# Performance work log

Hardware: AMD Instinct MI355X
Metric: run time of the kernel (lower is better)

The kernel has to match this reference:

```python
import jax, jax.numpy as jnp
import numpy as np

N_NODES = 50000
N_EDGES = 800000
F_IN = 32
H = 128
N_REL = 4
MAX_DEG = 10
N_GRAPHS = 64
N_BLOCKS = 2


def setup_inputs() -> dict:
    key = jax.random.key(0)
    ks = jax.random.split(key, 20)
    s = 0.05
    return {
        "x": jax.random.normal(ks[0], (N_NODES, F_IN), jnp.float32),
        "edge_index": jax.random.randint(ks[1], (2, N_EDGES), 0, N_NODES, dtype=jnp.int32),
        "edge_attr": jax.random.randint(ks[2], (N_EDGES,), 0, N_REL, dtype=jnp.int32),
        "batch_idx": jnp.sort(jax.random.randint(ks[3], (N_NODES,), 0, N_GRAPHS, dtype=jnp.int32)),
        "embed_W": jax.random.normal(ks[4], (F_IN, H), jnp.float32) * s,
        "embed_b": jax.random.normal(ks[5], (H,), jnp.float32) * s,
        "rgcn_Wrel": jax.random.normal(ks[6], (N_BLOCKS, N_REL, H, H), jnp.float32) * s,
        "rgcn_Wroot": jax.random.normal(ks[7], (N_BLOCKS, H, H), jnp.float32) * s,
        "rgcn_b": jax.random.normal(ks[8], (N_BLOCKS, H), jnp.float32) * s,
        "mf_Wl": jax.random.normal(ks[9], (N_BLOCKS, MAX_DEG + 1, H, H), jnp.float32) * s,
        "mf_bl": jax.random.normal(ks[10], (N_BLOCKS, MAX_DEG + 1, H), jnp.float32) * s,
        "mf_Wr": jax.random.normal(ks[11], (N_BLOCKS, MAX_DEG + 1, H, H), jnp.float32) * s,
        "lin1_W": jax.random.normal(ks[12], (H, H), jnp.float32) * s,
        "lin1_b": jax.random.normal(ks[13], (H,), jnp.float32) * s,
        "lin2_W": jax.random.normal(ks[14], (H, 1), jnp.float32) * s,
        "lin2_b": jax.random.normal(ks[15], (1,), jnp.float32) * s,
    }


def _rgcn(x, src, dst, rel, Wrel, Wroot, b):
    # PyG RGCNConv with default aggr='mean': per-relation mean over incoming
    # edges, then per-relation weight, plus root transform and bias.
    seg = dst * N_REL + rel  # composite segment id: (node, relation)
    agg = jax.ops.segment_sum(x[src], seg, num_segments=N_NODES * N_REL)
    cnt = jax.ops.segment_sum(jnp.ones((seg.shape[0],), x.dtype), seg,
                              num_segments=N_NODES * N_REL)
    agg = (agg / jnp.maximum(cnt, 1.0)[:, None]).reshape(N_NODES, N_REL, H)
    return jnp.einsum('nrh,rho->no', agg, Wrel) + x @ Wroot + b


def _mfconv(x, src, dst, Wl, bl, Wr):
    # PyG MFConv: sum-aggregate neighbors, then per-degree-bucket linear heads
    # (degree = in-degree clamped to MAX_DEG); lin_r applied to root x (no bias).
    h = jax.ops.segment_sum(x[src], dst, num_segments=N_NODES)  # [N,H]
    deg = jax.ops.segment_sum(jnp.ones((src.shape[0],), jnp.int32), dst,
                              num_segments=N_NODES)
    deg = jnp.minimum(deg, MAX_DEG)  # [N]
    # out_all: [D+1, N, H] candidate outputs, one per degree bucket
    out_all = (jnp.einsum('nh,dho->dno', h, Wl)
               + jnp.einsum('nh,dho->dno', x, Wr)
               + bl[:, None, :])
    return jnp.take_along_axis(out_all, deg[None, :, None], axis=0)[0]


def reference(x, edge_index, edge_attr, batch_idx, embed_W, embed_b,
              rgcn_Wrel, rgcn_Wroot, rgcn_b, mf_Wl, mf_bl, mf_Wr,
              lin1_W, lin1_b, lin2_W, lin2_b):
    src, dst = edge_index[0], edge_index[1]
    h = x @ embed_W + embed_b
    for blk in range(N_BLOCKS):
        if blk > 0:  # first block uses Identity instead of ReLU
            h = jax.nn.relu(h)
        h = _rgcn(h, src, dst, edge_attr, rgcn_Wrel[blk], rgcn_Wroot[blk], rgcn_b[blk])
        h = jax.nn.relu(h)
        h = _mfconv(h, src, dst, mf_Wl[blk], mf_bl[blk], mf_Wr[blk])
    g = jax.ops.segment_sum(h, batch_idx, num_segments=N_GRAPHS)  # global_add_pool
    g = jax.nn.relu(g @ lin1_W + lin1_b)
    return g @ lin2_W + lin2_b
```

## Files before the change

### kernel.cpp

```cpp
#include <hip/hip_runtime.h>
#include <hip/hip_bf16.h>

#define NRELS 4
#define MAXDEG 10
#define NBUCK 11
#define POOL_CHUNKS 8

typedef __attribute__((ext_vector_type(8))) short s16x8;
typedef __attribute__((ext_vector_type(4))) float f32x4;
typedef __attribute__((ext_vector_type(8))) unsigned short u16x8;

__device__ inline unsigned short f2b(float f) {
  __hip_bfloat16 h = __float2bfloat16(f);
  return *reinterpret_cast<unsigned short*>(&h);
}
__device__ inline float b2f(unsigned short u) {
  union { unsigned int i; float f; } v;
  v.i = ((unsigned int)u) << 16;
  return v.f;
}
__device__ inline float blo(unsigned int v) {
  union { unsigned int i; float f; } x;
  x.i = v << 16;
  return x.f;
}
__device__ inline float bhi(unsigned int v) {
  union { unsigned int i; float f; } x;
  x.i = v & 0xffff0000u;
  return x.f;
}

typedef __attribute__((address_space(3))) unsigned int lds_uint;
typedef __attribute__((address_space(1))) const unsigned int glob_uint;
__device__ __forceinline__ void gld_lds16(const void* g, void* l) {
  __builtin_amdgcn_global_load_lds((glob_uint*)g, (lds_uint*)l, 16, 0, 0);
}

__global__ __launch_bounds__(512) void coarse_count_scan(
    const int* __restrict__ dst, int* __restrict__ bhist, int* __restrict__ boff,
    int* __restrict__ bcur, int* __restrict__ done, int* __restrict__ perm, int permCap,
    int NB, int E, int nblocks) {
  __shared__ int lh[512];
  __shared__ int lastf;
  int t = threadIdx.x;
  lh[t] = 0;
  __syncthreads();
  for (int i = blockIdx.x * 512 + t; i < permCap; i += nblocks * 512) perm[i] = -1;
  int base = blockIdx.x * 4096;
  int lim = E - base;
  if (lim > 4096) lim = 4096;
  for (int i = t; i < lim; i += 512) atomicAdd(&lh[dst[base + i] >> 7], 1);
  __syncthreads();
  if (lh[t]) atomicAdd(&bhist[t], lh[t]);
  __threadfence();
  __syncthreads();
  if (t == 0) lastf = (atomicAdd(done, 1) == nblocks - 1) ? 1 : 0;
  __syncthreads();
  if (!lastf) return;
  int v = (t < NB) ? atomicAdd(&bhist[t], 0) : 0;
  lh[t] = v;
  __syncthreads();
  for (int o = 1; o < 512; o <<= 1) {
    int x = (t >= o) ? lh[t - o] : 0;
    __syncthreads();
    lh[t] += x;
    __syncthreads();
  }
  if (t < NB) {
    int st = lh[t] - v;
    boff[t] = st;
    bcur[t] = st;
  }
  if (t == 0) boff[NB] = E;
}

__global__ __launch_bounds__(512) void coarse_scatter(
    const int* __restrict__ src, const int* __restrict__ dst, const int* __restrict__ rel,
    int* __restrict__ bcur, uint2* __restrict__ ebuf, int E) {
  __shared__ int lhist[512];
  __shared__ int lstart[512];
  __shared__ int lcur[512];
  __shared__ int gbase[512];
  __shared__ uint2 stage[4096];
  int t = threadIdx.x;
  lhist[t] = 0;
  __syncthreads();
  int base = blockIdx.x * 4096;
  int lim = E - base;
  if (lim > 4096) lim = 4096;
  for (int i = t; i < lim; i += 512) atomicAdd(&lhist[dst[base + i] >> 7], 1);
  __syncthreads();
  int myc = lhist[t];
  lstart[t] = myc;
  __syncthreads();
  for (int o = 1; o < 512; o <<= 1) {
    int x = (t >= o) ? lstart[t - o] : 0;
    __syncthreads();
    lstart[t] += x;
    __syncthreads();
  }
  int incl = lstart[t];
  __syncthreads();
  lstart[t] = incl - myc;
  lcur[t] = 0;
  if (myc > 0) gbase[t] = atomicAdd(&bcur[t], myc);
  __syncthreads();
  for (int i = t; i < lim; i += 512) {
    int e = base + i;
    int d = dst[e];
    int b = d >> 7;
    int slot = lstart[b] + atomicAdd(&lcur[b], 1);
    stage[slot] = make_uint2((unsigned)(d * 4 + rel[e]), (unsigned)src[e]);
  }
  __syncthreads();
  for (int i = t; i < lim; i += 512) {
    uint2 val = stage[i];
    int b = (int)(val.x >> 9);
    ebuf[gbase[b] + (i - lstart[b])] = val;
  }
}

__global__ __launch_bounds__(512) void fine_place(
    const uint2* __restrict__ ebuf, const int* __restrict__ boff, int* __restrict__ cnt,
    int* __restrict__ seg_start, float* __restrict__ inv, int* __restrict__ deg,
    int* __restrict__ bucket, int* __restrict__ hist, int* __restrict__ csr, int NSEG) {
  __shared__ int lh[512];
  __shared__ int sc[512];
  __shared__ int lcur[512];
  __shared__ int lbh[16];
  int t = threadIdx.x;
  int b = blockIdx.x;
  lh[t] = 0;
  if (t < 16) lbh[t] = 0;
  __syncthreads();
  int s = boff[b], e = boff[b + 1];
  for (int i = s + t; i < e; i += 512) atomicAdd(&lh[ebuf[i].x & 511], 1);
  __syncthreads();
  int v = lh[t];
  sc[t] = v;
  __syncthreads();
  for (int o = 1; o < 512; o <<= 1) {
    int x = (t >= o) ? sc[t - o] : 0;
    __syncthreads();
    sc[t] += x;
    __syncthreads();
  }
  int gseg = b * 512 + t;
  int mystart = s + sc[t] - v;
  lcur[t] = mystart;
  if (gseg < NSEG) {
    cnt[gseg] = v;
    seg_start[gseg] = mystart;
    inv[gseg] = 1.0f / (float)(v > 1 ? v : 1);
    if ((t & 3) == 0) {
      int d = sc[t + 3] - sc[t] + v;
      int n = gseg >> 2;
      deg[n] = d;
      int bk = d < MAXDEG ? d : MAXDEG;
      bucket[n] = bk;
      atomicAdd(&lbh[bk], 1);
    }
  }
  __syncthreads();
  if (t < NBUCK && lbh[t]) atomicAdd(&hist[t], lbh[t]);
  for (int i = s + t; i < e; i += 512) {
    uint2 vv = ebuf[i];
    int pos = atomicAdd(&lcur[vv.x & 511], 1);
    csr[pos] = (int)vv.y;
  }
}

__global__ void build_perm(const int* __restrict__ bucket, const int* __restrict__ hist,
                           int* __restrict__ fill, int* __restrict__ perm, int N) {
  __shared__ int soff[NBUCK];
  if (threadIdx.x == 0) {
    int acc = 0;
    for (int b = 0; b < NBUCK; b++) {
      soff[b] = acc;
      acc += ((hist[b] + 63) >> 6) << 6;
    }
  }
  __syncthreads();
  int n = blockIdx.x * 256 + threadIdx.x;
  int b = (n < N) ? bucket[n] : -1;
  int lane = threadIdx.x & 63;
  for (int bb = 0; bb < NBUCK; bb++) {
    unsigned long long m = __ballot(b == bb);
    if (m == 0ULL) continue;
    int leader = __ffsll(m) - 1;
    int base = 0;
    if (lane == leader) base = atomicAdd(&fill[bb], __popcll(m));
    base = __shfl(base, leader);
    if (b == bb) {
      int idx = __popcll(m & ((1ULL << lane) - 1ULL));
      perm[soff[bb] + base + idx] = n;
    }
  }
}

__global__ __launch_bounds__(256) void embed_conv(
    const float* __restrict__ x, const float* __restrict__ embW,
    const float* __restrict__ bias, const float* __restrict__ Wrel,
    const float* __restrict__ Wroot, const float* __restrict__ Wl,
    const float* __restrict__ Wr, unsigned short* __restrict__ Bt,
    unsigned short* __restrict__ Btm, unsigned short* __restrict__ out, int N, int nbE) {
  if ((int)blockIdx.x >= nbE) {
    const int R1 = 2 * 128 * 640;
    const int R2 = R1 + 2 * 11 * 128 * 256;
    int t = (blockIdx.x - nbE) * 256 + threadIdx.x;
    if (t < R1) {
      int blk = t / 81920;
      int rem = t % 81920;
      int n = rem / 640;
      int k = rem % 640;
      float v;
      if (k < 512)
        v = Wrel[(size_t)blk * 65536 + (size_t)k * 128 + n];
      else
        v = Wroot[(size_t)blk * 16384 + (size_t)(k - 512) * 128 + n];
      Bt[t] = f2b(v);
    } else if (t < R2) {
      int t2 = t - R1;
      int k = t2 & 255;
      int n = (t2 >> 8) & 127;
      int bb = (t2 >> 15) % 11;
      int blk = t2 / (11 * 128 * 256);
      float v;
      if (k < 128)
        v = Wl[(((size_t)blk * 11 + bb) * 128 + k) * 128 + n];
      else
        v = Wr[(((size_t)blk * 11 + bb) * 128 + (k - 128)) * 128 + n];
      Btm[t2] = f2b(v);
    }
    return;
  }
  __shared__ unsigned char As[64 * 80];
  __shared__ unsigned char Bs[128 * 80];
  int t = threadIdx.x;
  int m0 = blockIdx.x * 64;
  {
    int r = t >> 2, s = t & 3;
    int gr = m0 + r;
    if (gr >= N) gr = N - 1;
    const float* xp = x + (size_t)gr * 32 + s * 8;
    float4 f0 = *(const float4*)xp;
    float4 f1 = *(const float4*)(xp + 4);
    u16x8 o;
    o[0] = f2b(f0.x); o[1] = f2b(f0.y); o[2] = f2b(f0.z); o[3] = f2b(f0.w);
    o[4] = f2b(f1.x); o[5] = f2b(f1.y); o[6] = f2b(f1.z); o[7] = f2b(f1.w);
    *(u16x8*)(As + r * 80 + s * 16) = o;
  }
  {
    int n = t >> 1, hf = t & 1;
    unsigned short tmp[16];
#pragma unroll
    for (int j = 0; j < 16; j++) tmp[j] = f2b(embW[(size_t)(hf * 16 + j) * 128 + n]);
    *(u16x8*)(Bs + n * 80 + hf * 32) = *(u16x8*)tmp;
    *(u16x8*)(Bs + n * 80 + hf * 32 + 16) = *(u16x8*)(tmp + 8);
  }
  __syncthreads();
  int lane = t & 63, wave = t >> 6;
  int row = lane & 15, quad = lane >> 4;
  int nh = wave * 32;
  f32x4 acc[2][4];
#pragma unroll
  for (int i = 0; i < 2; i++)
#pragma unroll
    for (int j = 0; j < 4; j++) acc[i][j] = (f32x4){0.f, 0.f, 0.f, 0.f};
  s16x8 af[4], bf[2];
#pragma unroll
  for (int mt = 0; mt < 4; mt++) {
    int R = mt * 16 + row;
    af[mt] = *(const s16x8*)(As + R * 80 + quad * 16);
  }
#pragma unroll
  for (int nt = 0; nt < 2; nt++) {
    int R = nh + nt * 16 + row;
    bf[nt] = *(const s16x8*)(Bs + R * 80 + quad * 16);
  }
#pragma unroll
  for (int nt = 0; nt < 2; nt++)
#pragma unroll
    for (int mt = 0; mt < 4; mt++)
      acc[nt][mt] = __builtin_amdgcn_mfma_f32_16x16x32_bf16(af[mt], bf[nt], acc[nt][mt], 0, 0, 0);
#pragma unroll
  for (int nt = 0; nt < 2; nt++) {
    int n = nh + nt * 16 + row;
    float bv = bias[n];
#pragma unroll
    for (int mt = 0; mt < 4; mt++) {
#pragma unroll
      for (int r4 = 0; r4 < 4; r4++) {
        int m = m0 + mt * 16 + quad * 4 + r4;
        if (m < N) out[(size_t)m * 128 + n] = f2b(acc[nt][mt][r4] + bv);
      }
    }
  }
}

__device__ __forceinline__ void acc8v(float* a, uint4 v) {
  a[0] += blo(v.x); a[1] += bhi(v.x);
  a[2] += blo(v.y); a[3] += bhi(v.y);
  a[4] += blo(v.z); a[5] += bhi(v.z);
  a[6] += blo(v.w); a[7] += bhi(v.w);
}

__device__ __forceinline__ void gather_seg(const unsigned short* __restrict__ hb,
                                           const int* __restrict__ csr, int st, int cn,
                                           int chunk, float* a) {
  const unsigned short* hq = hb + chunk * 16;
  int i = 0;
  for (; i + 2 <= cn; i += 2) {
    int p0 = csr[st + i], p1 = csr[st + i + 1];
    const uint4* r0 = (const uint4*)(hq + (size_t)p0 * 128);
    const uint4* r1 = (const uint4*)(hq + (size_t)p1 * 128);
    uint4 v00 = r0[0], v01 = r0[1];
    uint4 v10 = r1[0], v11 = r1[1];
    acc8v(a + 0, v00); acc8v(a + 8, v01);
    acc8v(a + 0, v10); acc8v(a + 8, v11);
  }
  if (i < cn) {
    const uint4* r0 = (const uint4*)(hq + (size_t)csr[st + i] * 128);
    acc8v(a + 0, r0[0]); acc8v(a + 8, r0[1]);
  }
}

__device__ __forceinline__ void write_frag(unsigned char* Ag, int ln, int chunk,
                                           const float* a, float w) {
  int s = chunk >> 2;
#pragma unroll
  for (int h = 0; h < 2; h++) {
    int c = (((chunk & 3) * 2 + h)) ^ (ln & 7);
    const float* p = a + h * 8;
    uint4 o;
    o.x = (unsigned int)f2b(p[0] * w) | ((unsigned int)f2b(p[1] * w) << 16);
    o.y = (unsigned int)f2b(p[2] * w) | ((unsigned int)f2b(p[3] * w) << 16);
    o.z = (unsigned int)f2b(p[4] * w) | ((unsigned int)f2b(p[5] * w) << 16);
    o.w = (unsigned int)f2b(p[6] * w) | ((unsigned int)f2b(p[7] * w) << 16);
    *(uint4*)(Ag + s * 8192 + ln * 128 + (c << 4)) = o;
  }
}

__device__ __forceinline__ void gemm_tile_gB(const unsigned char* Areg, const char* Bp,
                                             int strideB, int row, int quad, int nh,
                                             f32x4 acc[2][4]) {
#pragma unroll
  for (int s = 0; s < 2; s++) {
#pragma unroll
    for (int ks = 0; ks < 2; ks++) {
      int cch = ks * 4 + quad;
      s16x8 af[4], bf[2];
#pragma unroll
      for (int mt = 0; mt < 4; mt++) {
        int R = mt * 16 + row;
        af[mt] = *(const s16x8*)(Areg + s * 8192 + R * 128 + ((cch ^ (R & 7)) << 4));
      }
#pragma unroll
      for (int nt = 0; nt < 2; nt++) {
        int R = nh + nt * 16 + row;
        bf[nt] = *(const s16x8*)(Bp + (size_t)R * strideB + s * 128 + cch * 16);
      }
#pragma unroll
      for (int nt = 0; nt < 2; nt++)
#pragma unroll
        for (int mt = 0; mt < 4; mt++)
          acc[nt][mt] = __builtin_amdgcn_mfma_f32_16x16x32_bf16(af[mt], bf[nt], acc[nt][mt], 0, 0, 0);
    }
  }
}

__global__ __launch_bounds__(256) void rgcn_fused(
    const unsigned short* __restrict__ hb, const int* __restrict__ csr,
    const int* __restrict__ seg_start, const int* __restrict__ cnt,
    const float* __restrict__ inv, const int* __restrict__ perm,
    const unsigned short* __restrict__ Bt, const float* __restrict__ bias,
    unsigned short* __restrict__ out) {
  __shared__ unsigned char Ag0[16384];
  __shared__ unsigned char Ag1[16384];
  __shared__ int nodes[64];
  int t = threadIdx.x;
  int m0 = blockIdx.x * 64;
  if (t < 64) nodes[t] = perm[m0 + t];
  __syncthreads();
  int lane = t & 63, wave = t >> 6;
  int row = lane & 15, quad = lane >> 4;
  int nh = wave * 32;
  int chunk = t & 7, lnb = t >> 3;
  f32x4 acc[2][4];
#pragma unroll
  for (int i = 0; i < 2; i++)
#pragma unroll
    for (int j = 0; j < 4; j++) acc[i][j] = (f32x4){0.f, 0.f, 0.f, 0.f};

#pragma unroll
  for (int rp = 0; rp < 4; rp += 2) {
#pragma unroll
    for (int pp = 0; pp < 2; pp++) {
      int ln = pp * 32 + lnb;
      int nd = nodes[ln];
      float a0[16], a1[16];
#pragma unroll
      for (int j = 0; j < 16; j++) { a0[j] = 0.f; a1[j] = 0.f; }
      float w0 = 1.f, w1 = 1.f;
      if (nd >= 0) {
        int sb = nd * 4 + rp;
        int2 st2 = *(const int2*)(seg_start + sb);
        int2 cn2 = *(const int2*)(cnt + sb);
        float2 w2 = *(const float2*)(inv + sb);
        w0 = w2.x; w1 = w2.y;
        gather_seg(hb, csr, st2.x, cn2.x, chunk, a0);
        gather_seg(hb, csr, st2.y, cn2.y, chunk, a1);
      }
      write_frag(Ag0, ln, chunk, a0, w0);
      write_frag(Ag1, ln, chunk, a1, w1);
    }
    __syncthreads();
    gemm_tile_gB(Ag0, (const char*)Bt + rp * 256, 1280, row, quad, nh, acc);
    gemm_tile_gB(Ag1, (const char*)Bt + (rp + 1) * 256, 1280, row, quad, nh, acc);
    __syncthreads();
  }
#pragma unroll
  for (int s = 0; s < 2; s++)
#pragma unroll
    for (int p = 0; p < 2; p++) {
      int o = s * 8192 + p * 4096 + t * 16;
      int r = (o >> 7) & 63, c = ((o >> 4) & 7) ^ (r & 7);
      int nd = nodes[r];
      if (nd < 0) nd = 0;
      gld_lds16((const char*)hb + (size_t)nd * 256 + s * 128 + c * 16, Ag0 + o);
    }
  __syncthreads();
  gemm_tile_gB(Ag0, (const char*)Bt + 1024, 1280, row, quad, nh, acc);
#pragma unroll
  for (int nt = 0; nt < 2; nt++) {
    int n = nh + nt * 16 + row;
    float bv = bias[n];
#pragma unroll
    for (int mt = 0; mt < 4; mt++) {
#pragma unroll
      for (int r4 = 0; r4 < 4; r4++) {
        int nd = nodes[mt * 16 + quad * 4 + r4];
        if (nd >= 0) out[(size_t)nd * 128 + n] = f2b(fmaxf(acc[nt][mt][r4] + bv, 0.f));
      }
    }
  }
}

__global__ __launch_bounds__(256) void mf_fused(
    const unsigned short* __restrict__ hb, const int* __restrict__ csr,
    const int* __restrict__ seg_start, const int* __restrict__ deg,
    const int* __restrict__ perm, const int* __restrict__ hist,
    const unsigned short* __restrict__ Bt, const float* __restrict__ bl,
    unsigned short* __restrict__ out, int relu_out) {
  __shared__ unsigned char Ag[16384];
  __shared__ unsigned char Ar[16384];
  __shared__ int nodes[64];
  __shared__ int soff[NBUCK + 1];
  int t = threadIdx.x;
  int m0 = blockIdx.x * 64;
  if (t == 0) {
    int a2 = 0;
    for (int b2 = 0; b2 < NBUCK; b2++) {
      soff[b2] = a2;
      a2 += ((hist[b2] + 63) >> 6) << 6;
    }
    soff[NBUCK] = a2;
  }
  if (t < 64) nodes[t] = perm[m0 + t];
  __syncthreads();
  if (m0 >= soff[NBUCK]) return;
  int b = 0;
  while (b < 10 && m0 >= soff[b + 1]) b++;
  const char* Bb = (const char*)(Bt + (size_t)b * 128 * 256);
  int lane = t & 63, wave = t >> 6;
  int row = lane & 15, quad = lane >> 4;
  int nh = wave * 32;
  int chunk = t & 7, lnb = t >> 3;
#pragma unroll
  for (int s = 0; s < 2; s++)
#pragma unroll
    for (int p = 0; p < 2; p++) {
      int o = s * 8192 + p * 4096 + t * 16;
      int r = (o >> 7) & 63, c = ((o >> 4) & 7) ^ (r & 7);
      int nd = nodes[r];
      if (nd < 0) nd = 0;
      gld_lds16((const char*)hb + (size_t)nd * 256 + s * 128 + c * 16, Ar + o);
    }
  f32x4 acc[2][4];
#pragma unroll
  for (int i = 0; i < 2; i++)
#pragma unroll
    for (int j = 0; j < 4; j++) acc[i][j] = (f32x4){0.f, 0.f, 0.f, 0.f};
#pragma unroll
  for (int pp = 0; pp < 2; pp++) {
    int ln = pp * 32 + lnb;
    int nd = nodes[ln];
    float a[16];
#pragma unroll
    for (int j = 0; j < 16; j++) a[j] = 0.f;
    if (nd >= 0) gather_seg(hb, csr, seg_start[nd * 4], deg[nd], chunk, a);
    write_frag(Ag, ln, chunk, a, 1.f);
  }
  __syncthreads();
  gemm_tile_gB(Ag, Bb, 512, row, quad, nh, acc);
  gemm_tile_gB(Ar, Bb + 256, 512, row, quad, nh, acc);
  const float* bb = bl + b * 128;
#pragma unroll
  for (int nt = 0; nt < 2; nt++) {
    int n = nh + nt * 16 + row;
    float bv = bb[n];
#pragma unroll
    for (int mt = 0; mt < 4; mt++) {
#pragma unroll
      for (int r4 = 0; r4 < 4; r4++) {
        int nd = nodes[mt * 16 + quad * 4 + r4];
        if (nd >= 0) {
          float v = acc[nt][mt][r4] + bv;
          if (relu_out) v = fmaxf(v, 0.f);
          out[(size_t)nd * 128 + n] = f2b(v);
        }
      }
    }
  }
}

__global__ void pool2(const unsigned short* __restrict__ h, const int* __restrict__ batch,
                      float* __restrict__ g, int N, int G) {
  int gr = blockIdx.x / POOL_CHUNKS;
  int ck = blockIdx.x % POOL_CHUNKS;
  int t = threadIdx.x;
  int lane = t & 63, grp = t >> 6;
  int lo = 0, hi = N;
  while (lo < hi) {
    int m = (lo + hi) >> 1;
    if (batch[m] < gr) lo = m + 1; else hi = m;
  }
  int s = lo;
  lo = s; hi = N;
  while (lo < hi) {
    int m = (lo + hi) >> 1;
    if (batch[m] < gr + 1) lo = m + 1; else hi = m;
  }
  int e = lo;
  int len = e - s;
  int a = s + (int)(((long long)len * ck) / POOL_CHUNKS);
  int b = s + (int)(((long long)len * (ck + 1)) / POOL_CHUNKS);
  float s0 = 0.f, s1 = 0.f;
  for (int n = a + grp; n < b; n += 2) {
    unsigned int v = *(const unsigned int*)(h + (size_t)n * 128 + lane * 2);
    s0 += blo(v);
    s1 += bhi(v);
  }
  if (b > a + grp) {
    atomicAdd(&g[gr * 128 + lane * 2], s0);
    atomicAdd(&g[gr * 128 + lane * 2 + 1], s1);
  }
}

__global__ void head_kernel(const float* __restrict__ g, const float* __restrict__ W1,
                            const float* __restrict__ b1, const float* __restrict__ W2,
                            const float* __restrict__ b2, float* __restrict__ out) {
  int bg = blockIdx.x;
  int o = threadIdx.x;
  __shared__ float gs[128];
  __shared__ float red[128];
  gs[o] = g[bg * 128 + o];
  __syncthreads();
  float acc = b1[o];
  for (int k = 0; k < 128; k++) acc += gs[k] * W1[k * 128 + o];
  acc = fmaxf(acc, 0.f);
  red[o] = acc * W2[o];
  __syncthreads();
  for (int s = 64; s > 0; s >>= 1) {
    if (o < s) red[o] += red[o + s];
    __syncthreads();
  }
  if (o == 0) out[bg] = red[0] + b2[0];
}

extern "C" void kernel_launch(void* const* d_in, const int* in_sizes, int n_in,
                              void* d_out, int out_size, void* d_ws, size_t ws_size,
                              hipStream_t stream) {
  const float* x = (const float*)d_in[0];
  const int* ei = (const int*)d_in[1];
  const int* ea = (const int*)d_in[2];
  const int* batch = (const int*)d_in[3];
  const float* embW = (const float*)d_in[4];
  const float* embB = (const float*)d_in[5];
  const float* Wrel = (const float*)d_in[6];
  const float* Wroot = (const float*)d_in[7];
  const float* rb = (const float*)d_in[8];
  const float* Wl = (const float*)d_in[9];
  const float* bl = (const float*)d_in[10];
  const float* Wr = (const float*)d_in[11];
  const float* l1W = (const float*)d_in[12];
  const float* l1b = (const float*)d_in[13];
  const float* l2W = (const float*)d_in[14];
  const float* l2b = (const float*)d_in[15];
  float* out = (float*)d_out;

  int N = in_sizes[0] / 32;
  int E = in_sizes[2];
  int G = out_size;
  int NSEG = N * 4;
  int NB = (N + 127) >> 7;

  char* p = (char*)d_ws;
  auto alloc = [&](size_t bytes) {
    char* r = p;
    p += (bytes + 255) & ~(size_t)255;
    return r;
  };
  int permCap = ((N + 63) / 64 + NBUCK) * 64;
  unsigned short* h_bf = (unsigned short*)alloc((size_t)N * 128 * 2);
  unsigned short* h2_bf = (unsigned short*)alloc((size_t)N * 128 * 2);
  unsigned short* Btr = (unsigned short*)alloc((size_t)2 * 128 * 640 * 2);
  unsigned short* Btm = (unsigned short*)alloc((size_t)2 * 11 * 128 * 256 * 2);
  float* inv = (float*)alloc((size_t)NSEG * 4);
  int* cnt = (int*)alloc((size_t)NSEG * 4);
  int* seg_start = (int*)alloc((size_t)NSEG * 4);
  int* csr = (int*)alloc((size_t)E * 4);
  uint2* ebuf = (uint2*)alloc((size_t)E * 8);
  int* deg = (int*)alloc((size_t)N * 4);
  int* bucket = (int*)alloc((size_t)N * 4);
  int* perm = (int*)alloc((size_t)permCap * 4);
  int* boff = (int*)alloc(516 * 4);
  int* bcur = (int*)alloc(512 * 4);
  size_t zeroBytes = 8192 + (size_t)G * 128 * 4;
  char* zb = alloc(zeroBytes);
  int* bhist = (int*)zb;
  int* hist = (int*)(zb + 4096);
  int* fill = (int*)(zb + 4224);
  int* done = (int*)(zb + 4352);
  float* g = (float*)(zb + 8192);

  (void)hipMemsetAsync(zb, 0, zeroBytes, stream);

  const int* src = ei;
  const int* dst = ei + E;

  int sblocks = (E + 4095) / 4096;
  coarse_count_scan<<<sblocks, 512, 0, stream>>>(dst, bhist, boff, bcur, done, perm, permCap,
                                                 NB, E, sblocks);
  coarse_scatter<<<sblocks, 512, 0, stream>>>(src, dst, ea, bcur, ebuf, E);
  fine_place<<<NB, 512, 0, stream>>>(ebuf, boff, cnt, seg_start, inv, deg, bucket, hist, csr,
                                     NSEG);
  build_perm<<<(N + 255) / 256, 256, 0, stream>>>(bucket, hist, fill, perm, N);

  int nbE = (N + 63) / 64;
  int convBlocks = (2 * 128 * 640 + 2 * 11 * 128 * 256 + 255) / 256;
  embed_conv<<<nbE + convBlocks, 256, 0, stream>>>(x, embW, embB, Wrel, Wroot, Wl, Wr, Btr,
                                                   Btm, h_bf, N, nbE);

  int mfblocks = permCap / 64;
  for (int blk = 0; blk < 2; blk++) {
    rgcn_fused<<<mfblocks, 256, 0, stream>>>(h_bf, csr, seg_start, cnt, inv, perm,
                                             Btr + (size_t)blk * 81920, rb + blk * 128,
                                             h2_bf);
    mf_fused<<<mfblocks, 256, 0, stream>>>(h2_bf, csr, seg_start, deg, perm, hist,
                                           Btm + (size_t)blk * 11 * 128 * 256,
                                           bl + (size_t)blk * 11 * 128, h_bf,
                                           (blk == 0) ? 1 : 0);
  }
  pool2<<<G * POOL_CHUNKS, 128, 0, stream>>>(h_bf, batch, g, N, G);
  head_kernel<<<G, 128, 0, stream>>>(g, l1W, l1b, l2W, l2b, out);
}
```

Measured before the change: 456.4 us.

## Pipeline RGCN gather with MFMA via ping-pong LDS and finer degree buckets

The RGCN fused kernel now gathers the next relation's neighbour aggregates into registers while the MFMA GEMM runs on the previous relation's LDS tile. Two LDS buffers alternate so each relation needs one barrier instead of two. Separately, nodes whose degree is at or above the clamp are split into extra sort buckets (up to 32) by actual degree, so the gather work within a 64-node tile is more uniform. Those extra buckets still map to the same weight head. The costs are more register pressure from holding gathered values across the GEMM, and more padding in the permutation.

```diff
diff --git a/kernel.cpp b/kernel.cpp
--- a/kernel.cpp
+++ b/kernel.cpp
@@ -4,6 +4,7 @@
 #define NRELS 4
 #define MAXDEG 10
 #define NBUCK 11
+#define NBUCKF 32
 #define POOL_CHUNKS 8
 
 typedef __attribute__((ext_vector_type(8))) short s16x8;
@@ -127,11 +128,11 @@
   __shared__ int lh[512];
   __shared__ int sc[512];
   __shared__ int lcur[512];
-  __shared__ int lbh[16];
+  __shared__ int lbh[NBUCKF];
   int t = threadIdx.x;
   int b = blockIdx.x;
   lh[t] = 0;
-  if (t < 16) lbh[t] = 0;
+  if (t < NBUCKF) lbh[t] = 0;
   __syncthreads();
   int s = boff[b], e = boff[b + 1];
   for (int i = s + t; i < e; i += 512) atomicAdd(&lh[ebuf[i].x & 511], 1);
@@ -156,13 +157,14 @@
       int d = sc[t + 3] - sc[t] + v;
       int n = gseg >> 2;
       deg[n] = d;
-      int bk = d < MAXDEG ? d : MAXDEG;
+      int ext = d - MAXDEG;
+      int bk = d < MAXDEG ? d : (MAXDEG + (ext < NBUCKF - 1 - MAXDEG ? ext : NBUCKF - 1 - MAXDEG));
       bucket[n] = bk;
       atomicAdd(&lbh[bk], 1);
     }
   }
   __syncthreads();
-  if (t < NBUCK && lbh[t]) atomicAdd(&hist[t], lbh[t]);
+  if (t < NBUCKF && lbh[t]) atomicAdd(&hist[t], lbh[t]);
   for (int i = s + t; i < e; i += 512) {
     uint2 vv = ebuf[i];
     int pos = atomicAdd(&lcur[vv.x & 511], 1);
@@ -172,10 +174,10 @@
 
 __global__ void build_perm(const int* __restrict__ bucket, const int* __restrict__ hist,
                            int* __restrict__ fill, int* __restrict__ perm, int N) {
-  __shared__ int soff[NBUCK];
+  __shared__ int soff[NBUCKF];
   if (threadIdx.x == 0) {
     int acc = 0;
-    for (int b = 0; b < NBUCK; b++) {
+    for (int b = 0; b < NBUCKF; b++) {
       soff[b] = acc;
       acc += ((hist[b] + 63) >> 6) << 6;
     }
@@ -184,7 +186,7 @@
   int n = blockIdx.x * 256 + threadIdx.x;
   int b = (n < N) ? bucket[n] : -1;
   int lane = threadIdx.x & 63;
-  for (int bb = 0; bb < NBUCK; bb++) {
+  for (int bb = 0; bb < NBUCKF; bb++) {
     unsigned long long m = __ballot(b == bb);
     if (m == 0ULL) continue;
     int leader = __ffsll(m) - 1;
@@ -375,8 +377,8 @@
     const float* __restrict__ inv, const int* __restrict__ perm,
     const unsigned short* __restrict__ Bt, const float* __restrict__ bias,
     unsigned short* __restrict__ out) {
-  __shared__ unsigned char Ag0[16384];
-  __shared__ unsigned char Ag1[16384];
+  __shared__ unsigned char AgA[16384];
+  __shared__ unsigned char AgB[16384];
   __shared__ int nodes[64];
   int t = threadIdx.x;
   int m0 = blockIdx.x * 64;
@@ -386,39 +388,51 @@
   int row = lane & 15, quad = lane >> 4;
   int nh = wave * 32;
   int chunk = t & 7, lnb = t >> 3;
+  int ln0 = lnb, ln1 = 32 + lnb;
+  int nd0 = nodes[ln0], nd1 = nodes[ln1];
   f32x4 acc[2][4];
 #pragma unroll
   for (int i = 0; i < 2; i++)
 #pragma unroll
     for (int j = 0; j < 4; j++) acc[i][j] = (f32x4){0.f, 0.f, 0.f, 0.f};
 
-#pragma unroll
-  for (int rp = 0; rp < 4; rp += 2) {
-#pragma unroll
-    for (int pp = 0; pp < 2; pp++) {
-      int ln = pp * 32 + lnb;
-      int nd = nodes[ln];
-      float a0[16], a1[16];
-#pragma unroll
-      for (int j = 0; j < 16; j++) { a0[j] = 0.f; a1[j] = 0.f; }
-      float w0 = 1.f, w1 = 1.f;
-      if (nd >= 0) {
-        int sb = nd * 4 + rp;
-        int2 st2 = *(const int2*)(seg_start + sb);
-        int2 cn2 = *(const int2*)(cnt + sb);
-        float2 w2 = *(const float2*)(inv + sb);
-        w0 = w2.x; w1 = w2.y;
-        gather_seg(hb, csr, st2.x, cn2.x, chunk, a0);
-        gather_seg(hb, csr, st2.y, cn2.y, chunk, a1);
-      }
-      write_frag(Ag0, ln, chunk, a0, w0);
-      write_frag(Ag1, ln, chunk, a1, w1);
-    }
-    __syncthreads();
-    gemm_tile_gB(Ag0, (const char*)Bt + rp * 256, 1280, row, quad, nh, acc);
-    gemm_tile_gB(Ag1, (const char*)Bt + (rp + 1) * 256, 1280, row, quad, nh, acc);
-    __syncthreads();
-  }
+  float a0[16], a1[16];
+  float w0, w1;
+  auto gather2 = [&](int rel) {
+#pragma unroll
+    for (int j = 0; j < 16; j++) { a0[j] = 0.f; a1[j] = 0.f; }
+    w0 = 1.f; w1 = 1.f;
+    if (nd0 >= 0) {
+      int sid = nd0 * 4 + rel;
+      w0 = inv[sid];
+      gather_seg(hb, csr, seg_start[sid], cnt[sid], chunk, a0);
+    }
+    if (nd1 >= 0) {
+      int sid = nd1 * 4 + rel;
+      w1 = inv[sid];
+      gather_seg(hb, csr, seg_start[sid], cnt[sid], chunk, a1);
+    }
+  };
+
+  gather2(0);
+  write_frag(AgA, ln0, chunk, a0, w0);
+  write_frag(AgA, ln1, chunk, a1, w1);
+  __syncthreads();
+  gather2(1);
+  gemm_tile_gB(AgA, (const char*)Bt + 0, 1280, row, quad, nh, acc);
+  write_frag(AgB, ln0, chunk, a0, w0);
+  write_frag(AgB, ln1, chunk, a1, w1);
+  __syncthreads();
+  gather2(2);
+  gemm_tile_gB(AgB, (const char*)Bt + 256, 1280, row, quad, nh, acc);
+  write_frag(AgA, ln0, chunk, a0, w0);
+  write_frag(AgA, ln1, chunk, a1, w1);
+  __syncthreads();
+  gather2(3);
+  gemm_tile_gB(AgA, (const char*)Bt + 512, 1280, row, quad, nh, acc);
+  write_frag(AgB, ln0, chunk, a0, w0);
+  write_frag(AgB, ln1, chunk, a1, w1);
+  __syncthreads();
 #pragma unroll
   for (int s = 0; s < 2; s++)
 #pragma unroll
@@ -427,10 +441,11 @@
       int r = (o >> 7) & 63, c = ((o >> 4) & 7) ^ (r & 7);
       int nd = nodes[r];
       if (nd < 0) nd = 0;
-      gld_lds16((const char*)hb + (size_t)nd * 256 + s * 128 + c * 16, Ag0 + o);
-    }
-  __syncthreads();
-  gemm_tile_gB(Ag0, (const char*)Bt + 1024, 1280, row, quad, nh, acc);
+      gld_lds16((const char*)hb + (size_t)nd * 256 + s * 128 + c * 16, AgA + o);
+    }
+  gemm_tile_gB(AgB, (const char*)Bt + 768, 1280, row, quad, nh, acc);
+  __syncthreads();
+  gemm_tile_gB(AgA, (const char*)Bt + 1024, 1280, row, quad, nh, acc);
 #pragma unroll
   for (int nt = 0; nt < 2; nt++) {
     int n = nh + nt * 16 + row;
@@ -455,22 +470,23 @@
   __shared__ unsigned char Ag[16384];
   __shared__ unsigned char Ar[16384];
   __shared__ int nodes[64];
-  __shared__ int soff[NBUCK + 1];
+  __shared__ int soff[NBUCKF + 1];
   int t = threadIdx.x;
   int m0 = blockIdx.x * 64;
   if (t == 0) {
     int a2 = 0;
-    for (int b2 = 0; b2 < NBUCK; b2++) {
+    for (int b2 = 0; b2 < NBUCKF; b2++) {
       soff[b2] = a2;
       a2 += ((hist[b2] + 63) >> 6) << 6;
     }
-    soff[NBUCK] = a2;
+    soff[NBUCKF] = a2;
   }
   if (t < 64) nodes[t] = perm[m0 + t];
   __syncthreads();
-  if (m0 >= soff[NBUCK]) return;
-  int b = 0;
-  while (b < 10 && m0 >= soff[b + 1]) b++;
+  if (m0 >= soff[NBUCKF]) return;
+  int f = 0;
+  while (f < NBUCKF - 1 && m0 >= soff[f + 1]) f++;
+  int b = f < MAXDEG ? f : MAXDEG;
   const char* Bb = (const char*)(Bt + (size_t)b * 128 * 256);
   int lane = t & 63, wave = t >> 6;
   int row = lane & 15, quad = lane >> 4;
@@ -611,7 +627,7 @@
     p += (bytes + 255) & ~(size_t)255;
     return r;
   };
-  int permCap = ((N + 63) / 64 + NBUCK) * 64;
+  int permCap = ((N + 63) / 64 + NBUCKF) * 64;
   unsigned short* h_bf = (unsigned short*)alloc((size_t)N * 128 * 2);
   unsigned short* h2_bf = (unsigned short*)alloc((size_t)N * 128 * 2);
   unsigned short* Btr = (unsigned short*)alloc((size_t)2 * 128 * 640 * 2);
```

Measured after the change: 607.2 us. +33.0%, slower.
